# Kernel tuning notes

Hardware: AMD Instinct MI355X
Metric: run time of the kernel (lower is better)

The kernel has to match this reference:

```python
import jax, jax.numpy as jnp
import numpy as np

B, S, D, H, F, E, K = 2, 2048, 1024, 16, 4096, 8, 2
DK = D // H


def _ln(x, g, b, eps=1e-5):
    m = jnp.mean(x, axis=-1, keepdims=True)
    v = jnp.var(x, axis=-1, keepdims=True)
    return (x - m) * jax.lax.rsqrt(v + eps) * g + b


def _silu(x):
    return x * jax.nn.sigmoid(x)


def _gated_proj(x, w1, b1, w2, b2):
    # SiLU(x W1 + b1) * (x W2 + b2)
    return _silu(x @ w1 + b1) * (x @ w2 + b2)


def setup_inputs() -> dict:
    key = jax.random.key(0)
    ks = jax.random.split(key, 32)

    def n(k, shape, s=0.02):
        return jax.random.normal(k, shape, jnp.float32) * s

    inp = {
        "x": jax.random.normal(ks[0], (B, S, D), jnp.float32),
        "wq1": n(ks[1], (D, D)), "bq1": jnp.zeros((D,), jnp.float32),
        "wq2": n(ks[2], (D, D)), "bq2": jnp.zeros((D,), jnp.float32),
        "wk1": n(ks[3], (D, D)), "bk1": jnp.zeros((D,), jnp.float32),
        "wk2": n(ks[4], (D, D)), "bk2": jnp.zeros((D,), jnp.float32),
        "wv1": n(ks[5], (D, D)), "bv1": jnp.zeros((D,), jnp.float32),
        "wv2": n(ks[6], (D, D)), "bv2": jnp.zeros((D,), jnp.float32),
        "wo": n(ks[7], (D, D)), "bo": jnp.zeros((D,), jnp.float32),
        "ln1_g": jnp.ones((D,), jnp.float32), "ln1_b": jnp.zeros((D,), jnp.float32),
        "ln2_g": jnp.ones((D,), jnp.float32), "ln2_b": jnp.zeros((D,), jnp.float32),
        "gate_w": n(ks[8], (D, E)), "gate_b": jnp.zeros((E,), jnp.float32),
        "e_w1": n(ks[9], (E, D, F)), "e_b1": jnp.zeros((E, F), jnp.float32),
        "e_w2": n(ks[10], (E, F, D)), "e_b2": jnp.zeros((E, D), jnp.float32),
        "e_w3": n(ks[11], (E, D, F)), "e_b3": jnp.zeros((E, F), jnp.float32),
    }
    return inp


def _attention(x2, wq1, bq1, wq2, bq2, wk1, bk1, wk2, bk2,
               wv1, bv1, wv2, bv2, wo, bo, eps=1e-6):
    q = _gated_proj(x2, wq1, bq1, wq2, bq2).reshape(B, S, H, DK)
    k = _gated_proj(x2, wk1, bk1, wk2, bk2).reshape(B, S, H, DK)
    v = _gated_proj(x2, wv1, bv1, wv2, bv2).reshape(B, S, H, DK)
    phi_q = jax.nn.elu(q) + 1.0
    phi_k = jax.nn.elu(k) + 1.0
    # kv: [B,H,DK,DK] -- associative reordering of linear attention
    kv = jnp.einsum("bshd,bshe->bhde", phi_k, v)
    ksum = jnp.sum(phi_k, axis=1)  # [B,H,DK]
    qksum = jnp.einsum("bshd,bhd->bsh", phi_q, ksum)
    num = jnp.einsum("bshd,bhde->bshe", phi_q, kv)
    out = num / (qksum[..., None] + eps)  # [B,S,H,DK]
    return out.reshape(B, S, D) @ wo + bo


def _moe(x2, gate_w, gate_b, e_w1, e_b1, e_w2, e_b2, e_w3, e_b3):
    gate_probs = jax.nn.softmax(x2 @ gate_w + gate_b, axis=-1)  # [B,S,E]
    topv, topi = jax.lax.top_k(gate_probs, K)  # [B,S,K]
    topv = topv / (jnp.sum(topv, axis=-1, keepdims=True) + 1e-6)
    # combine weight per expert: [B,S,E]
    comb = jnp.sum(jax.nn.one_hot(topi, E, dtype=x2.dtype) * topv[..., None], axis=-2)
    out = jnp.zeros_like(x2)
    for e in range(E):  # small fixed expert count
        h = _silu(x2 @ e_w1[e] + e_b1[e]) * (x2 @ e_w3[e] + e_b3[e])
        out = out + (h @ e_w2[e] + e_b2[e]) * comb[..., e, None]
    return out


def reference(x, wq1, bq1, wq2, bq2, wk1, bk1, wk2, bk2, wv1, bv1, wv2, bv2,
              wo, bo, ln1_g, ln1_b, ln2_g, ln2_b, gate_w, gate_b,
              e_w1, e_b1, e_w2, e_b2, e_w3, e_b3):
    x2 = _ln(x, ln1_g, ln1_b)
    x = x + _attention(x2, wq1, bq1, wq2, bq2, wk1, bk1, wk2, bk2,
                       wv1, bv1, wv2, bv2, wo, bo)
    x2 = _ln(x, ln2_g, ln2_b)
    x = x + _moe(x2, gate_w, gate_b, e_w1, e_b1, e_w2, e_b2, e_w3, e_b3)
    return x
```

## Files before the change

### kernel.cpp

```cpp
#include <hip/hip_runtime.h>
#include <cstdint>
#include <cstddef>

typedef __bf16 bf16;
typedef bf16  bf16x8 __attribute__((ext_vector_type(8)));
typedef bf16  bf16x4 __attribute__((ext_vector_type(4)));
typedef float f32x4  __attribute__((ext_vector_type(4)));

#define B_ 2
#define S_ 2048
#define D_ 1024
#define H_ 16
#define F_ 4096
#define E_ 8
#define T_ (B_*S_)

__device__ __forceinline__ void gl16(const bf16* g, bf16* l) {
    __builtin_amdgcn_global_load_lds(
        (const __attribute__((address_space(1))) void*)g,
        (__attribute__((address_space(3))) void*)l, 16, 0, 0);
}

__global__ __launch_bounds__(256) void transpose_convert(const float* __restrict__ in,
                                                         bf16* __restrict__ out,
                                                         int R, int C) {
    __shared__ float tile[32][33];
    size_t mat = blockIdx.z;
    in  += mat * (size_t)R * C;
    out += mat * (size_t)R * C;
    int c0 = blockIdx.x * 32, r0 = blockIdx.y * 32;
    for (int i = threadIdx.y; i < 32; i += 8)
        tile[i][threadIdx.x] = in[(size_t)(r0 + i) * C + c0 + threadIdx.x];
    __syncthreads();
    for (int i = threadIdx.y; i < 32; i += 8)
        out[(size_t)(c0 + i) * R + r0 + threadIdx.x] = (bf16)tile[threadIdx.x][i];
}

__global__ __launch_bounds__(256) void ln_kernel(const float* __restrict__ xin,
                                                 const float* __restrict__ gam,
                                                 const float* __restrict__ bet,
                                                 bf16* __restrict__ obf,
                                                 float* __restrict__ of32) {
    int row = blockIdx.x, tid = threadIdx.x;
    const float4* xr = (const float4*)(xin + (size_t)row * D_);
    float4 v = xr[tid];
    float s  = v.x + v.y + v.z + v.w;
    float s2 = v.x*v.x + v.y*v.y + v.z*v.z + v.w*v.w;
    #pragma unroll
    for (int o = 1; o < 64; o <<= 1) { s += __shfl_xor(s, o); s2 += __shfl_xor(s2, o); }
    __shared__ float red[8];
    int wave = tid >> 6, lane = tid & 63;
    if (lane == 0) { red[wave] = s; red[4 + wave] = s2; }
    __syncthreads();
    s  = red[0] + red[1] + red[2] + red[3];
    s2 = red[4] + red[5] + red[6] + red[7];
    float m   = s * (1.0f / D_);
    float var = s2 * (1.0f / D_) - m * m;
    float rs  = rsqrtf(var + 1e-5f);
    float4 gv = ((const float4*)gam)[tid];
    float4 bv = ((const float4*)bet)[tid];
    float y0 = (v.x - m) * rs * gv.x + bv.x;
    float y1 = (v.y - m) * rs * gv.y + bv.y;
    float y2 = (v.z - m) * rs * gv.z + bv.z;
    float y3 = (v.w - m) * rs * gv.w + bv.w;
    bf16x4 ov; ov[0] = (bf16)y0; ov[1] = (bf16)y1; ov[2] = (bf16)y2; ov[3] = (bf16)y3;
    *(bf16x4*)(obf + (size_t)row * D_ + tid * 4) = ov;
    if (of32) {
        float4 o4; o4.x = y0; o4.y = y1; o4.z = y2; o4.w = y3;
        ((float4*)of32)[(size_t)row * (D_/4) + tid] = o4;
    }
}


template<int MODE>
__global__ __launch_bounds__(256) void gemm_dual128(const bf16* __restrict__ A,
                                                    const bf16* __restrict__ B1,
                                                    const bf16* __restrict__ B2,
                                                    const float* __restrict__ bias1,
                                                    const float* __restrict__ bias2,
                                                    float* __restrict__ out,
                                                    int N, int K) {
    __shared__ alignas(16) bf16 As [128 * 32];
    __shared__ alignas(16) bf16 B1s[64 * 32];
    __shared__ alignas(16) bf16 B2s[64 * 32];
    const int tid = threadIdx.x;
    const int wave = tid >> 6, lane = tid & 63;
    const int nb = blockIdx.x, mb = blockIdx.y;
    const int wr = (wave >> 1) * 64;
    const int wc = (wave & 1) * 32;
    const int fr = lane & 15, fk = (lane >> 4) * 8;
    const int srow = lane >> 2;
    const int scol = (lane & 3) * 8;
    const int cA0 = wave, cA1 = wave + 4;
    const bf16* Ap0 = A  + (size_t)(mb * 128 + cA0 * 16 + srow) * K + scol;
    const bf16* Ap1 = A  + (size_t)(mb * 128 + cA1 * 16 + srow) * K + scol;
    const bf16* B1p = B1 + (size_t)(nb * 64 + wave * 16 + srow) * K + scol;
    const bf16* B2p = B2 + (size_t)(nb * 64 + wave * 16 + srow) * K + scol;
    bf16* lA0 = As  + cA0 * 512;
    bf16* lA1 = As  + cA1 * 512;
    bf16* lB1 = B1s + wave * 512;
    bf16* lB2 = B2s + wave * 512;
    f32x4 acc1[4][2] = {};
    f32x4 acc2[4][2] = {};
    for (int k0 = 0; k0 < K; k0 += 32) {
        gl16(Ap0 + k0, lA0);
        gl16(Ap1 + k0, lA1);
        gl16(B1p + k0, lB1);
        gl16(B2p + k0, lB2);
        __syncthreads();
        bf16x8 af[4];
        #pragma unroll
        for (int mi = 0; mi < 4; mi++)
            af[mi] = *(const bf16x8*)&As[(wr + mi * 16 + fr) * 32 + fk];
        #pragma unroll
        for (int ni = 0; ni < 2; ni++) {
            bf16x8 b1f = *(const bf16x8*)&B1s[(wc + ni * 16 + fr) * 32 + fk];
            bf16x8 b2f = *(const bf16x8*)&B2s[(wc + ni * 16 + fr) * 32 + fk];
            #pragma unroll
            for (int mi = 0; mi < 4; mi++) {
                acc1[mi][ni] = __builtin_amdgcn_mfma_f32_16x16x32_bf16(af[mi], b1f, acc1[mi][ni], 0, 0, 0);
                acc2[mi][ni] = __builtin_amdgcn_mfma_f32_16x16x32_bf16(af[mi], b2f, acc2[mi][ni], 0, 0, 0);
            }
        }
        __syncthreads();
    }
    const int col = lane & 15, rowq = (lane >> 4) * 4;
    #pragma unroll
    for (int ni = 0; ni < 2; ni++) {
        int gn = nb * 64 + wc + ni * 16 + col;
        float bb1 = bias1[gn], bb2 = bias2[gn];
        #pragma unroll
        for (int mi = 0; mi < 4; mi++) {
            #pragma unroll
            for (int r = 0; r < 4; r++) {
                int gm = mb * 128 + wr + mi * 16 + rowq + r;
                float p1 = acc1[mi][ni][r] + bb1;
                float p2 = acc2[mi][ni][r] + bb2;
                float g = (p1 / (1.0f + expf(-p1))) * p2;
                size_t idx = (size_t)gm * N + gn;
                if (MODE == 0) {
                    float e = g > 0.0f ? g : expm1f(g);
                    out[idx] = e + 1.0f;
                } else {
                    out[idx] = g;
                }
            }
        }
    }
}

__global__ __launch_bounds__(256) void gemm_single128(const bf16* __restrict__ A,
                                                      const bf16* __restrict__ Bt,
                                                      float* __restrict__ out,
                                                      int N, int K) {
    __shared__ alignas(16) bf16 As[128 * 32];
    __shared__ alignas(16) bf16 Bs[64 * 32];
    const int tid = threadIdx.x;
    const int wave = tid >> 6, lane = tid & 63;
    const int nb = blockIdx.x, mb = blockIdx.y;
    const int wr = (wave >> 1) * 64, wc = (wave & 1) * 32;
    const int fr = lane & 15, fk = (lane >> 4) * 8;
    const int srow = lane >> 2, scol = (lane & 3) * 8;
    const int cA0 = wave, cA1 = wave + 4;
    const bf16* Ap0 = A  + (size_t)(mb * 128 + cA0 * 16 + srow) * K + scol;
    const bf16* Ap1 = A  + (size_t)(mb * 128 + cA1 * 16 + srow) * K + scol;
    const bf16* Bp  = Bt + (size_t)(nb * 64 + wave * 16 + srow) * K + scol;
    bf16* lA0 = As + cA0 * 512;
    bf16* lA1 = As + cA1 * 512;
    bf16* lB  = Bs + wave * 512;
    f32x4 acc[4][2] = {};
    for (int k0 = 0; k0 < K; k0 += 32) {
        gl16(Ap0 + k0, lA0);
        gl16(Ap1 + k0, lA1);
        gl16(Bp  + k0, lB);
        __syncthreads();
        bf16x8 af[4];
        #pragma unroll
        for (int mi = 0; mi < 4; mi++)
            af[mi] = *(const bf16x8*)&As[(wr + mi * 16 + fr) * 32 + fk];
        #pragma unroll
        for (int ni = 0; ni < 2; ni++) {
            bf16x8 bf = *(const bf16x8*)&Bs[(wc + ni * 16 + fr) * 32 + fk];
            #pragma unroll
            for (int mi = 0; mi < 4; mi++)
                acc[mi][ni] = __builtin_amdgcn_mfma_f32_16x16x32_bf16(af[mi], bf, acc[mi][ni], 0, 0, 0);
        }
        __syncthreads();
    }
    const int col = lane & 15, rowq = (lane >> 4) * 4;
    #pragma unroll
    for (int ni = 0; ni < 2; ni++) {
        int gn = nb * 64 + wc + ni * 16 + col;
        #pragma unroll
        for (int mi = 0; mi < 4; mi++)
            #pragma unroll
            for (int r = 0; r < 4; r++) {
                int gm = mb * 128 + wr + mi * 16 + rowq + r;
                out[(size_t)gm * N + gn] = acc[mi][ni][r];
            }
    }
}

__global__ __launch_bounds__(256) void gemm_dual_moe128(const bf16* __restrict__ A,
                                                        const bf16* __restrict__ B1all,
                                                        const bf16* __restrict__ B2all,
                                                        const float* __restrict__ b1all,
                                                        const float* __restrict__ b2all,
                                                        const int* __restrict__ list,
                                                        const int* __restrict__ counts,
                                                        const int* __restrict__ ebase,
                                                        bf16* __restrict__ outAct,
                                                        int N, int K) {
    const int e = blockIdx.z;
    const int cnt = counts[e * 64];
    const int mb = blockIdx.y;
    if (mb * 128 >= cnt) return;
    __shared__ alignas(16) bf16 As [128 * 32];
    __shared__ alignas(16) bf16 B1s[64 * 32];
    __shared__ alignas(16) bf16 B2s[64 * 32];
    const bf16* B1 = B1all + (size_t)e * N * K;
    const bf16* B2 = B2all + (size_t)e * N * K;
    const float* bias1 = b1all + (size_t)e * N;
    const float* bias2 = b2all + (size_t)e * N;
    const int tid = threadIdx.x;
    const int wave = tid >> 6, lane = tid & 63;
    const int nb = blockIdx.x;
    const int wr = (wave >> 1) * 64, wc = (wave & 1) * 32;
    const int fr = lane & 15, fk = (lane >> 4) * 8;
    const int srow = lane >> 2, scol = (lane & 3) * 8;
    const int cA0 = wave, cA1 = wave + 4;
    int gr0 = mb * 128 + cA0 * 16 + srow;
    int gr1 = mb * 128 + cA1 * 16 + srow;
    int tok0 = list[e * T_ + (gr0 < cnt ? gr0 : cnt - 1)];
    int tok1 = list[e * T_ + (gr1 < cnt ? gr1 : cnt - 1)];
    const bf16* Ap0 = A  + (size_t)tok0 * K + scol;
    const bf16* Ap1 = A  + (size_t)tok1 * K + scol;
    const bf16* B1p = B1 + (size_t)(nb * 64 + wave * 16 + srow) * K + scol;
    const bf16* B2p = B2 + (size_t)(nb * 64 + wave * 16 + srow) * K + scol;
    bf16* lA0 = As  + cA0 * 512;
    bf16* lA1 = As  + cA1 * 512;
    bf16* lB1 = B1s + wave * 512;
    bf16* lB2 = B2s + wave * 512;
    f32x4 acc1[4][2] = {};
    f32x4 acc2[4][2] = {};
    for (int k0 = 0; k0 < K; k0 += 32) {
        gl16(Ap0 + k0, lA0);
        gl16(Ap1 + k0, lA1);
        gl16(B1p + k0, lB1);
        gl16(B2p + k0, lB2);
        __syncthreads();
        bf16x8 af[4];
        #pragma unroll
        for (int mi = 0; mi < 4; mi++)
            af[mi] = *(const bf16x8*)&As[(wr + mi * 16 + fr) * 32 + fk];
        #pragma unroll
        for (int ni = 0; ni < 2; ni++) {
            bf16x8 b1f = *(const bf16x8*)&B1s[(wc + ni * 16 + fr) * 32 + fk];
            bf16x8 b2f = *(const bf16x8*)&B2s[(wc + ni * 16 + fr) * 32 + fk];
            #pragma unroll
            for (int mi = 0; mi < 4; mi++) {
                acc1[mi][ni] = __builtin_amdgcn_mfma_f32_16x16x32_bf16(af[mi], b1f, acc1[mi][ni], 0, 0, 0);
                acc2[mi][ni] = __builtin_amdgcn_mfma_f32_16x16x32_bf16(af[mi], b2f, acc2[mi][ni], 0, 0, 0);
            }
        }
        __syncthreads();
    }
    const int col = lane & 15, rowq = (lane >> 4) * 4;
    const size_t rbase = (size_t)ebase[e] + mb * 128;
    #pragma unroll
    for (int ni = 0; ni < 2; ni++) {
        int gn = nb * 64 + wc + ni * 16 + col;
        float bb1 = bias1[gn], bb2 = bias2[gn];
        #pragma unroll
        for (int mi = 0; mi < 4; mi++)
            #pragma unroll
            for (int r = 0; r < 4; r++) {
                int lm = wr + mi * 16 + rowq + r;
                float p1 = acc1[mi][ni][r] + bb1;
                float p2 = acc2[mi][ni][r] + bb2;
                float g = (p1 / (1.0f + expf(-p1))) * p2;
                outAct[(rbase + lm) * N + gn] = (bf16)g;
            }
    }
}

__global__ __launch_bounds__(256) void gemm_down_moe128(const bf16* __restrict__ Act,
                                                        const bf16* __restrict__ Ball,
                                                        const float* __restrict__ ball,
                                                        const int* __restrict__ list,
                                                        const float* __restrict__ wgt,
                                                        const int* __restrict__ counts,
                                                        const int* __restrict__ ebase,
                                                        float* __restrict__ out,
                                                        int N, int K) {
    const int e = blockIdx.z;
    const int cnt = counts[e * 64];
    const int mb = blockIdx.y;
    if (mb * 128 >= cnt) return;
    __shared__ alignas(16) bf16 As[128 * 32];
    __shared__ alignas(16) bf16 Bs[64 * 32];
    const bf16* A  = Act + (size_t)ebase[e] * K;
    const bf16* Bt = Ball + (size_t)e * N * K;
    const float* bias = ball + (size_t)e * N;
    const int tid = threadIdx.x;
    const int wave = tid >> 6, lane = tid & 63;
    const int nb = blockIdx.x;
    const int wr = (wave >> 1) * 64, wc = (wave & 1) * 32;
    const int fr = lane & 15, fk = (lane >> 4) * 8;
    const int srow = lane >> 2, scol = (lane & 3) * 8;
    const int cA0 = wave, cA1 = wave + 4;
    const bf16* Ap0 = A  + (size_t)(mb * 128 + cA0 * 16 + srow) * K + scol;
    const bf16* Ap1 = A  + (size_t)(mb * 128 + cA1 * 16 + srow) * K + scol;
    const bf16* Bp  = Bt + (size_t)(nb * 64 + wave * 16 + srow) * K + scol;
    bf16* lA0 = As + cA0 * 512;
    bf16* lA1 = As + cA1 * 512;
    bf16* lB  = Bs + wave * 512;
    f32x4 acc[4][2] = {};
    for (int k0 = 0; k0 < K; k0 += 32) {
        gl16(Ap0 + k0, lA0);
        gl16(Ap1 + k0, lA1);
        gl16(Bp  + k0, lB);
        __syncthreads();
        bf16x8 af[4];
        #pragma unroll
        for (int mi = 0; mi < 4; mi++)
            af[mi] = *(const bf16x8*)&As[(wr + mi * 16 + fr) * 32 + fk];
        #pragma unroll
        for (int ni = 0; ni < 2; ni++) {
            bf16x8 bf = *(const bf16x8*)&Bs[(wc + ni * 16 + fr) * 32 + fk];
            #pragma unroll
            for (int mi = 0; mi < 4; mi++)
                acc[mi][ni] = __builtin_amdgcn_mfma_f32_16x16x32_bf16(af[mi], bf, acc[mi][ni], 0, 0, 0);
        }
        __syncthreads();
    }
    const int col = lane & 15, rowq = (lane >> 4) * 4;
    #pragma unroll
    for (int ni = 0; ni < 2; ni++) {
        int gn = nb * 64 + wc + ni * 16 + col;
        float bb = bias[gn];
        #pragma unroll
        for (int mi = 0; mi < 4; mi++)
            #pragma unroll
            for (int r = 0; r < 4; r++) {
                int gm = mb * 128 + wr + mi * 16 + rowq + r;
                if (gm < cnt) {
                    int tok = list[e * T_ + gm];
                    float w = wgt[e * T_ + gm];
                    atomicAdd(&out[(size_t)tok * N + gn], (acc[mi][ni][r] + bb) * w);
                }
            }
    }
}

__global__ __launch_bounds__(256) void attn_kv_part(const float* __restrict__ phi_k,
                                                    const float* __restrict__ vv_g,
                                                    float* __restrict__ kvp,
                                                    float* __restrict__ ksp) {
    int bh = blockIdx.x;
    int chunk = blockIdx.y;
    int b = bh >> 4, h = bh & 15;
    __shared__ float pk[64][68];
    __shared__ float vv[64][68];
    int tid = threadIdx.x;
    int d0 = (tid >> 4) * 4;
    int e0 = (tid & 15) * 4;
    float acc[4][4] = {};
    float ks[4] = {};
    int sbeg = chunk * (S_ / 8);
    for (int s0 = sbeg; s0 < sbeg + S_ / 8; s0 += 64) {
        __syncthreads();
        for (int i = tid; i < 1024; i += 256) {
            int r = i >> 4, c4 = i & 15;
            size_t base = ((size_t)(b * S_ + s0 + r) * D_ + h * 64);
            ((float4*)&pk[r][0])[c4] = ((const float4*)(phi_k + base))[c4];
            ((float4*)&vv[r][0])[c4] = ((const float4*)(vv_g + base))[c4];
        }
        __syncthreads();
        for (int s = 0; s < 64; s++) {
            float a0 = pk[s][d0], a1 = pk[s][d0+1], a2 = pk[s][d0+2], a3 = pk[s][d0+3];
            float b0 = vv[s][e0], b1 = vv[s][e0+1], b2 = vv[s][e0+2], b3 = vv[s][e0+3];
            acc[0][0] += a0*b0; acc[0][1] += a0*b1; acc[0][2] += a0*b2; acc[0][3] += a0*b3;
            acc[1][0] += a1*b0; acc[1][1] += a1*b1; acc[1][2] += a1*b2; acc[1][3] += a1*b3;
            acc[2][0] += a2*b0; acc[2][1] += a2*b1; acc[2][2] += a2*b2; acc[2][3] += a2*b3;
            acc[3][0] += a3*b0; acc[3][1] += a3*b1; acc[3][2] += a3*b2; acc[3][3] += a3*b3;
            if ((tid & 15) == 0) { ks[0] += a0; ks[1] += a1; ks[2] += a2; ks[3] += a3; }
        }
    }
    float* kvo = kvp + ((size_t)bh * 8 + chunk) * 4096;
    for (int i = 0; i < 4; i++)
        for (int j = 0; j < 4; j++)
            kvo[(d0 + i) * 64 + e0 + j] = acc[i][j];
    if ((tid & 15) == 0)
        for (int i = 0; i < 4; i++) ksp[((size_t)bh * 8 + chunk) * 64 + d0 + i] = ks[i];
}

__global__ __launch_bounds__(256) void attn_kv_reduce(const float* __restrict__ kvp,
                                                      const float* __restrict__ ksp,
                                                      float* __restrict__ kv,
                                                      float* __restrict__ ksum) {
    int bh = blockIdx.x;
    int tid = threadIdx.x;
    #pragma unroll
    for (int i = 0; i < 4; i++) {
        int idx = i * 256 + tid;
        float4 s = {0, 0, 0, 0};
        #pragma unroll
        for (int c = 0; c < 8; c++) {
            float4 p = ((const float4*)(kvp + ((size_t)bh * 8 + c) * 4096))[idx];
            s.x += p.x; s.y += p.y; s.z += p.z; s.w += p.w;
        }
        ((float4*)(kv + (size_t)bh * 4096))[idx] = s;
    }
    if (tid < 64) {
        float s = 0;
        #pragma unroll
        for (int c = 0; c < 8; c++) s += ksp[((size_t)bh * 8 + c) * 64 + tid];
        ksum[bh * 64 + tid] = s;
    }
}

__global__ __launch_bounds__(256) void attn_num(const float* __restrict__ phi_q,
                                                const float* __restrict__ kv,
                                                const float* __restrict__ ksum,
                                                bf16* __restrict__ outb) {
    int bh = blockIdx.y;
    int b = bh >> 4, h = bh & 15;
    int s0 = blockIdx.x * 64;
    __shared__ float kvs[64][64];
    __shared__ float pqs[64][68];
    __shared__ float kss[64];
    int tid = threadIdx.x;
    const float* kvsrc = kv + (size_t)bh * 4096;
    for (int i = tid; i < 1024; i += 256) ((float4*)kvs)[i] = ((const float4*)kvsrc)[i];
    if (tid < 16) ((float4*)kss)[tid] = ((const float4*)(ksum + bh * 64))[tid];
    for (int i = tid; i < 1024; i += 256) {
        int r = i >> 4, c4 = i & 15;
        ((float4*)&pqs[r][0])[c4] =
            ((const float4*)(phi_q + ((size_t)(b * S_ + s0 + r) * D_ + h * 64)))[c4];
    }
    __syncthreads();
    int tok = tid >> 2;
    int e0  = (tid & 3) * 16;
    float acc[16] = {};
    float qk = 0.0f;
    for (int d = 0; d < 64; d++) {
        float pq = pqs[tok][d];
        qk += pq * kss[d];
        #pragma unroll
        for (int ei = 0; ei < 16; ei++) acc[ei] += pq * kvs[d][e0 + ei];
    }
    float inv = 1.0f / (qk + 1e-6f);
    int t = b * S_ + s0 + tok;
    bf16* op = outb + (size_t)t * D_ + h * 64 + e0;
    #pragma unroll
    for (int ei = 0; ei < 16; ei++) op[ei] = (bf16)(acc[ei] * inv);
}

__global__ __launch_bounds__(256) void residual_kernel(const float* __restrict__ x,
                                                       const float* __restrict__ prod,
                                                       const float* __restrict__ bo,
                                                       float* __restrict__ x1,
                                                       float* __restrict__ outp) {
    int i = blockIdx.x * 256 + threadIdx.x;
    float4 xv = ((const float4*)x)[i];
    float4 pv = ((const float4*)prod)[i];
    float4 bv = ((const float4*)bo)[i & 255];
    float4 r;
    r.x = xv.x + pv.x + bv.x; r.y = xv.y + pv.y + bv.y;
    r.z = xv.z + pv.z + bv.z; r.w = xv.w + pv.w + bv.w;
    ((float4*)x1)[i] = r;
    ((float4*)outp)[i] = r;
}

__global__ void zero_counts(int* counts) {
    counts[threadIdx.x] = 0;
}

__global__ void expert_bases(const int* __restrict__ counts, int* __restrict__ ebase) {
    if (threadIdx.x == 0) {
        int b = 0;
        #pragma unroll
        for (int e = 0; e < E_; e++) {
            ebase[e] = b;
            b += (counts[e * 64] + 127) & ~127;
        }
    }
}

__global__ __launch_bounds__(256) void gate_kernel(const float* __restrict__ x2f,
                                                   const float* __restrict__ gw,
                                                   const float* __restrict__ gb,
                                                   int* __restrict__ counts,
                                                   int* __restrict__ list,
                                                   float* __restrict__ wgt) {
    int tid = threadIdx.x;
    int wave = tid >> 6, lane = tid & 63;
    int t = blockIdx.x * 4 + wave;
    const float* xr = x2f + (size_t)t * D_;
    float le[8] = {};
    for (int i = 0; i < 16; i++) {
        int d = lane + i * 64;
        float xv = xr[d];
        const float4* g4 = (const float4*)(gw + (size_t)d * 8);
        float4 a = g4[0], b = g4[1];
        le[0] += xv * a.x; le[1] += xv * a.y; le[2] += xv * a.z; le[3] += xv * a.w;
        le[4] += xv * b.x; le[5] += xv * b.y; le[6] += xv * b.z; le[7] += xv * b.w;
    }
    #pragma unroll
    for (int o = 1; o < 64; o <<= 1)
        #pragma unroll
        for (int e = 0; e < 8; e++) le[e] += __shfl_xor(le[e], o);
    if (lane == 0) {
        float probs[8]; float mx = -1e30f;
        for (int e = 0; e < 8; e++) { le[e] += gb[e]; mx = fmaxf(mx, le[e]); }
        float s = 0.0f;
        for (int e = 0; e < 8; e++) { probs[e] = expf(le[e] - mx); s += probs[e]; }
        float invs = 1.0f / s;
        for (int e = 0; e < 8; e++) probs[e] *= invs;
        int i1 = 0; float v1 = probs[0];
        for (int e = 1; e < 8; e++) if (probs[e] > v1) { v1 = probs[e]; i1 = e; }
        int i2 = -1; float v2 = -1.0f;
        for (int e = 0; e < 8; e++) if (e != i1 && probs[e] > v2) { v2 = probs[e]; i2 = e; }
        float inv = 1.0f / (v1 + v2 + 1e-6f);
        int p1 = atomicAdd(&counts[i1 * 64], 1);
        list[i1 * T_ + p1] = t; wgt[i1 * T_ + p1] = v1 * inv;
        int p2 = atomicAdd(&counts[i2 * 64], 1);
        list[i2 * T_ + p2] = t; wgt[i2 * T_ + p2] = v2 * inv;
    }
}

extern "C" void kernel_launch(void* const* d_in, const int* in_sizes, int n_in,
                              void* d_out, int out_size, void* d_ws, size_t ws_size,
                              hipStream_t stream) {
    const float* x    = (const float*)d_in[0];
    const float* wq1  = (const float*)d_in[1];
    const float* bq1  = (const float*)d_in[2];
    const float* wq2  = (const float*)d_in[3];
    const float* bq2  = (const float*)d_in[4];
    const float* wk1  = (const float*)d_in[5];
    const float* bk1  = (const float*)d_in[6];
    const float* wk2  = (const float*)d_in[7];
    const float* bk2  = (const float*)d_in[8];
    const float* wv1  = (const float*)d_in[9];
    const float* bv1  = (const float*)d_in[10];
    const float* wv2  = (const float*)d_in[11];
    const float* bv2  = (const float*)d_in[12];
    const float* wo   = (const float*)d_in[13];
    const float* bo   = (const float*)d_in[14];
    const float* ln1g = (const float*)d_in[15];
    const float* ln1b = (const float*)d_in[16];
    const float* ln2g = (const float*)d_in[17];
    const float* ln2b = (const float*)d_in[18];
    const float* gw   = (const float*)d_in[19];
    const float* gb   = (const float*)d_in[20];
    const float* ew1  = (const float*)d_in[21];
    const float* eb1  = (const float*)d_in[22];
    const float* ew2  = (const float*)d_in[23];
    const float* eb2  = (const float*)d_in[24];
    const float* ew3  = (const float*)d_in[25];
    const float* eb3  = (const float*)d_in[26];
    float* out = (float*)d_out;

    char* wsb = (char*)d_ws;
    size_t off = 0;
    auto carve = [&](size_t bytes) -> char* {
        char* r = wsb + off;
        off = (off + bytes + 255) & ~(size_t)255;
        return r;
    };
    bf16* Wq1t = (bf16*)carve((size_t)D_ * D_ * 2);
    bf16* Wq2t = (bf16*)carve((size_t)D_ * D_ * 2);
    bf16* Wk1t = (bf16*)carve((size_t)D_ * D_ * 2);
    bf16* Wk2t = (bf16*)carve((size_t)D_ * D_ * 2);
    bf16* Wv1t = (bf16*)carve((size_t)D_ * D_ * 2);
    bf16* Wv2t = (bf16*)carve((size_t)D_ * D_ * 2);
    bf16* Wot  = (bf16*)carve((size_t)D_ * D_ * 2);
    bf16* We1t = (bf16*)carve((size_t)E_ * D_ * F_ * 2);
    bf16* We3t = (bf16*)carve((size_t)E_ * D_ * F_ * 2);
    bf16* We2t = (bf16*)carve((size_t)E_ * D_ * F_ * 2);
    bf16*  X2b  = (bf16*)carve((size_t)T_ * D_ * 2);
    float* PhiQ = (float*)carve((size_t)T_ * D_ * 4);
    float* PhiK = (float*)carve((size_t)T_ * D_ * 4);
    float* Vb   = (float*)carve((size_t)T_ * D_ * 4);
    float* KV   = (float*)carve((size_t)B_ * H_ * 64 * 64 * 4);
    float* KS   = (float*)carve((size_t)B_ * H_ * 64 * 4);
    float* KVp  = (float*)carve((size_t)B_ * H_ * 8 * 64 * 64 * 4);
    float* KSp  = (float*)carve((size_t)B_ * H_ * 8 * 64 * 4);
    bf16*  Attn = (bf16*)carve((size_t)T_ * D_ * 2);
    float* WoP  = (float*)carve((size_t)T_ * D_ * 4);
    float* X1   = (float*)carve((size_t)T_ * D_ * 4);
    bf16*  X2c  = (bf16*)carve((size_t)T_ * D_ * 2);
    int*   Cnt  = (int*)carve((size_t)E_ * 64 * 4);
    int*   List = (int*)carve((size_t)E_ * T_ * 4);
    float* Wgt  = (float*)carve((size_t)E_ * T_ * 4);
    int*   Ebase = (int*)carve((size_t)E_ * 4);
    bf16*  Act  = (bf16*)PhiQ;
    float* X2f  = WoP;

    dim3 tb32(32, 8);
    transpose_convert<<<dim3(32, 32, 1), tb32, 0, stream>>>(wq1, Wq1t, D_, D_);
    transpose_convert<<<dim3(32, 32, 1), tb32, 0, stream>>>(wq2, Wq2t, D_, D_);
    transpose_convert<<<dim3(32, 32, 1), tb32, 0, stream>>>(wk1, Wk1t, D_, D_);
    transpose_convert<<<dim3(32, 32, 1), tb32, 0, stream>>>(wk2, Wk2t, D_, D_);
    transpose_convert<<<dim3(32, 32, 1), tb32, 0, stream>>>(wv1, Wv1t, D_, D_);
    transpose_convert<<<dim3(32, 32, 1), tb32, 0, stream>>>(wv2, Wv2t, D_, D_);
    transpose_convert<<<dim3(32, 32, 1), tb32, 0, stream>>>(wo,  Wot,  D_, D_);
    transpose_convert<<<dim3(F_/32, D_/32, E_), tb32, 0, stream>>>(ew1, We1t, D_, F_);
    transpose_convert<<<dim3(F_/32, D_/32, E_), tb32, 0, stream>>>(ew3, We3t, D_, F_);
    transpose_convert<<<dim3(D_/32, F_/32, E_), tb32, 0, stream>>>(ew2, We2t, F_, D_);

    zero_counts<<<1, E_ * 64, 0, stream>>>(Cnt);

    ln_kernel<<<T_, 256, 0, stream>>>(x, ln1g, ln1b, X2b, nullptr);

    gemm_dual128<0><<<dim3(D_/64, T_/128), 256, 0, stream>>>(X2b, Wq1t, Wq2t, bq1, bq2, PhiQ, D_, D_);
    gemm_dual128<0><<<dim3(D_/64, T_/128), 256, 0, stream>>>(X2b, Wk1t, Wk2t, bk1, bk2, PhiK, D_, D_);
    gemm_dual128<1><<<dim3(D_/64, T_/128), 256, 0, stream>>>(X2b, Wv1t, Wv2t, bv1, bv2, Vb,   D_, D_);

    attn_kv_part<<<dim3(B_ * H_, 8), 256, 0, stream>>>(PhiK, Vb, KVp, KSp);
    attn_kv_reduce<<<B_ * H_, 256, 0, stream>>>(KVp, KSp, KV, KS);
    attn_num<<<dim3(S_/64, B_ * H_), 256, 0, stream>>>(PhiQ, KV, KS, Attn);

    gemm_single128<<<dim3(D_/64, T_/128), 256, 0, stream>>>(Attn, Wot, WoP, D_, D_);
    residual_kernel<<<T_ * D_ / 1024, 256, 0, stream>>>(x, WoP, bo, X1, out);

    ln_kernel<<<T_, 256, 0, stream>>>(X1, ln2g, ln2b, X2c, X2f);
    gate_kernel<<<T_ / 4, 256, 0, stream>>>(X2f, gw, gb, Cnt, List, Wgt);
    expert_bases<<<1, 64, 0, stream>>>(Cnt, Ebase);

    gemm_dual_moe128<<<dim3(F_/64, T_/128, E_), 256, 0, stream>>>(
        X2c, We1t, We3t, eb1, eb3, List, Cnt, Ebase, Act, F_, D_);
    gemm_down_moe128<<<dim3(D_/64, T_/128, E_), 256, 0, stream>>>(
        Act, We2t, eb2, List, Wgt, Cnt, Ebase, out, D_, F_);
}
```

Baseline: 1.153 ms.

## Double-buffer LDS in all GEMMs and widen single-B GEMM tiles to 128x128

```diff
diff --git a/kernel.cpp b/kernel.cpp
--- a/kernel.cpp
+++ b/kernel.cpp
@@ -80,42 +80,43 @@
                                                     const float* __restrict__ bias2,
                                                     float* __restrict__ out,
                                                     int N, int K) {
-    __shared__ alignas(16) bf16 As [128 * 32];
-    __shared__ alignas(16) bf16 B1s[64 * 32];
-    __shared__ alignas(16) bf16 B2s[64 * 32];
+    __shared__ alignas(16) bf16 As [2][128 * 32];
+    __shared__ alignas(16) bf16 B1s[2][64 * 32];
+    __shared__ alignas(16) bf16 B2s[2][64 * 32];
     const int tid = threadIdx.x;
     const int wave = tid >> 6, lane = tid & 63;
     const int nb = blockIdx.x, mb = blockIdx.y;
     const int wr = (wave >> 1) * 64;
     const int wc = (wave & 1) * 32;
     const int fr = lane & 15, fk = (lane >> 4) * 8;
-    const int srow = lane >> 2;
-    const int scol = (lane & 3) * 8;
-    const int cA0 = wave, cA1 = wave + 4;
-    const bf16* Ap0 = A  + (size_t)(mb * 128 + cA0 * 16 + srow) * K + scol;
-    const bf16* Ap1 = A  + (size_t)(mb * 128 + cA1 * 16 + srow) * K + scol;
+    const int srow = lane >> 2, scol = (lane & 3) * 8;
+    const int co = wave * 512;
+    const bf16* Ap0 = A  + (size_t)(mb * 128 + wave * 16 + srow) * K + scol;
+    const bf16* Ap1 = A  + (size_t)(mb * 128 + (wave + 4) * 16 + srow) * K + scol;
     const bf16* B1p = B1 + (size_t)(nb * 64 + wave * 16 + srow) * K + scol;
     const bf16* B2p = B2 + (size_t)(nb * 64 + wave * 16 + srow) * K + scol;
-    bf16* lA0 = As  + cA0 * 512;
-    bf16* lA1 = As  + cA1 * 512;
-    bf16* lB1 = B1s + wave * 512;
-    bf16* lB2 = B2s + wave * 512;
     f32x4 acc1[4][2] = {};
     f32x4 acc2[4][2] = {};
-    for (int k0 = 0; k0 < K; k0 += 32) {
-        gl16(Ap0 + k0, lA0);
-        gl16(Ap1 + k0, lA1);
-        gl16(B1p + k0, lB1);
-        gl16(B2p + k0, lB2);
-        __syncthreads();
+    gl16(Ap0, &As[0][co]);
+    gl16(Ap1, &As[0][co + 2048]);
+    gl16(B1p, &B1s[0][co]);
+    gl16(B2p, &B2s[0][co]);
+    __syncthreads();
+    int cur = 0;
+    for (int k0 = 32; k0 < K; k0 += 32) {
+        int nxt = cur ^ 1;
+        gl16(Ap0 + k0, &As[nxt][co]);
+        gl16(Ap1 + k0, &As[nxt][co + 2048]);
+        gl16(B1p + k0, &B1s[nxt][co]);
+        gl16(B2p + k0, &B2s[nxt][co]);
         bf16x8 af[4];
         #pragma unroll
         for (int mi = 0; mi < 4; mi++)
-            af[mi] = *(const bf16x8*)&As[(wr + mi * 16 + fr) * 32 + fk];
+            af[mi] = *(const bf16x8*)&As[cur][(wr + mi * 16 + fr) * 32 + fk];
         #pragma unroll
         for (int ni = 0; ni < 2; ni++) {
-            bf16x8 b1f = *(const bf16x8*)&B1s[(wc + ni * 16 + fr) * 32 + fk];
-            bf16x8 b2f = *(const bf16x8*)&B2s[(wc + ni * 16 + fr) * 32 + fk];
+            bf16x8 b1f = *(const bf16x8*)&B1s[cur][(wc + ni * 16 + fr) * 32 + fk];
+            bf16x8 b2f = *(const bf16x8*)&B2s[cur][(wc + ni * 16 + fr) * 32 + fk];
             #pragma unroll
             for (int mi = 0; mi < 4; mi++) {
                 acc1[mi][ni] = __builtin_amdgcn_mfma_f32_16x16x32_bf16(af[mi], b1f, acc1[mi][ni], 0, 0, 0);
@@ -123,6 +124,23 @@
             }
         }
         __syncthreads();
+        cur = nxt;
+    }
+    {
+        bf16x8 af[4];
+        #pragma unroll
+        for (int mi = 0; mi < 4; mi++)
+            af[mi] = *(const bf16x8*)&As[cur][(wr + mi * 16 + fr) * 32 + fk];
+        #pragma unroll
+        for (int ni = 0; ni < 2; ni++) {
+            bf16x8 b1f = *(const bf16x8*)&B1s[cur][(wc + ni * 16 + fr) * 32 + fk];
+            bf16x8 b2f = *(const bf16x8*)&B2s[cur][(wc + ni * 16 + fr) * 32 + fk];
+            #pragma unroll
+            for (int mi = 0; mi < 4; mi++) {
+                acc1[mi][ni] = __builtin_amdgcn_mfma_f32_16x16x32_bf16(af[mi], b1f, acc1[mi][ni], 0, 0, 0);
+                acc2[mi][ni] = __builtin_amdgcn_mfma_f32_16x16x32_bf16(af[mi], b2f, acc2[mi][ni], 0, 0, 0);
+            }
+        }
     }
     const int col = lane & 15, rowq = (lane >> 4) * 4;
     #pragma unroll
@@ -153,44 +171,65 @@
                                                       const bf16* __restrict__ Bt,
                                                       float* __restrict__ out,
                                                       int N, int K) {
-    __shared__ alignas(16) bf16 As[128 * 32];
-    __shared__ alignas(16) bf16 Bs[64 * 32];
+    __shared__ alignas(16) bf16 As[2][128 * 32];
+    __shared__ alignas(16) bf16 Bs[2][128 * 32];
     const int tid = threadIdx.x;
     const int wave = tid >> 6, lane = tid & 63;
     const int nb = blockIdx.x, mb = blockIdx.y;
-    const int wr = (wave >> 1) * 64, wc = (wave & 1) * 32;
+    const int wr = (wave >> 1) * 64, wc = (wave & 1) * 64;
     const int fr = lane & 15, fk = (lane >> 4) * 8;
     const int srow = lane >> 2, scol = (lane & 3) * 8;
-    const int cA0 = wave, cA1 = wave + 4;
-    const bf16* Ap0 = A  + (size_t)(mb * 128 + cA0 * 16 + srow) * K + scol;
-    const bf16* Ap1 = A  + (size_t)(mb * 128 + cA1 * 16 + srow) * K + scol;
-    const bf16* Bp  = Bt + (size_t)(nb * 64 + wave * 16 + srow) * K + scol;
-    bf16* lA0 = As + cA0 * 512;
-    bf16* lA1 = As + cA1 * 512;
-    bf16* lB  = Bs + wave * 512;
-    f32x4 acc[4][2] = {};
-    for (int k0 = 0; k0 < K; k0 += 32) {
-        gl16(Ap0 + k0, lA0);
-        gl16(Ap1 + k0, lA1);
-        gl16(Bp  + k0, lB);
+    const int co = wave * 512;
+    const bf16* Ap0 = A  + (size_t)(mb * 128 + wave * 16 + srow) * K + scol;
+    const bf16* Ap1 = A  + (size_t)(mb * 128 + (wave + 4) * 16 + srow) * K + scol;
+    const bf16* Bp0 = Bt + (size_t)(nb * 128 + wave * 16 + srow) * K + scol;
+    const bf16* Bp1 = Bt + (size_t)(nb * 128 + (wave + 4) * 16 + srow) * K + scol;
+    f32x4 acc[4][4] = {};
+    gl16(Ap0, &As[0][co]);
+    gl16(Ap1, &As[0][co + 2048]);
+    gl16(Bp0, &Bs[0][co]);
+    gl16(Bp1, &Bs[0][co + 2048]);
+    __syncthreads();
+    int cur = 0;
+    for (int k0 = 32; k0 < K; k0 += 32) {
+        int nxt = cur ^ 1;
+        gl16(Ap0 + k0, &As[nxt][co]);
+        gl16(Ap1 + k0, &As[nxt][co + 2048]);
+        gl16(Bp0 + k0, &Bs[nxt][co]);
+        gl16(Bp1 + k0, &Bs[nxt][co + 2048]);
+        bf16x8 af[4], bf[4];
+        #pragma unroll
+        for (int mi = 0; mi < 4; mi++)
+            af[mi] = *(const bf16x8*)&As[cur][(wr + mi * 16 + fr) * 32 + fk];
+        #pragma unroll
+        for (int ni = 0; ni < 4; ni++)
+            bf[ni] = *(const bf16x8*)&Bs[cur][(wc + ni * 16 + fr) * 32 + fk];
+        #pragma unroll
+        for (int ni = 0; ni < 4; ni++)
+            #pragma unroll
+            for (int mi = 0; mi < 4; mi++)
+                acc[mi][ni] = __builtin_amdgcn_mfma_f32_16x16x32_bf16(af[mi], bf[ni], acc[mi][ni], 0, 0, 0);
         __syncthreads();
-        bf16x8 af[4];
-        #pragma unroll
-        for (int mi = 0; mi < 4; mi++)
-            af[mi] = *(const bf16x8*)&As[(wr + mi * 16 + fr) * 32 + fk];
-        #pragma unroll
-        for (int ni = 0; ni < 2; ni++) {
-            bf16x8 bf = *(const bf16x8*)&Bs[(wc + ni * 16 + fr) * 32 + fk];
+        cur = nxt;
+    }
+    {
+        bf16x8 af[4], bf[4];
+        #pragma unroll
+        for (int mi = 0; mi < 4; mi++)
+            af[mi] = *(const bf16x8*)&As[cur][(wr + mi * 16 + fr) * 32 + fk];
+        #pragma unroll
+        for (int ni = 0; ni < 4; ni++)
+            bf[ni] = *(const bf16x8*)&Bs[cur][(wc + ni * 16 + fr) * 32 + fk];
+        #pragma unroll
+        for (int ni = 0; ni < 4; ni++)
             #pragma unroll
             for (int mi = 0; mi < 4; mi++)
-                acc[mi][ni] = __builtin_amdgcn_mfma_f32_16x16x32_bf16(af[mi], bf, acc[mi][ni], 0, 0, 0);
-        }
-        __syncthreads();
+                acc[mi][ni] = __builtin_amdgcn_mfma_f32_16x16x32_bf16(af[mi], bf[ni], acc[mi][ni], 0, 0, 0);
     }
     const int col = lane & 15, rowq = (lane >> 4) * 4;
     #pragma unroll
-    for (int ni = 0; ni < 2; ni++) {
-        int gn = nb * 64 + wc + ni * 16 + col;
+    for (int ni = 0; ni < 4; ni++) {
+        int gn = nb * 128 + wc + ni * 16 + col;
         #pragma unroll
         for (int mi = 0; mi < 4; mi++)
             #pragma unroll
@@ -215,9 +254,9 @@
     const int cnt = counts[e * 64];
     const int mb = blockIdx.y;
     if (mb * 128 >= cnt) return;
-    __shared__ alignas(16) bf16 As [128 * 32];
-    __shared__ alignas(16) bf16 B1s[64 * 32];
-    __shared__ alignas(16) bf16 B2s[64 * 32];
+    __shared__ alignas(16) bf16 As [2][128 * 32];
+    __shared__ alignas(16) bf16 B1s[2][64 * 32];
+    __shared__ alignas(16) bf16 B2s[2][64 * 32];
     const bf16* B1 = B1all + (size_t)e * N * K;
     const bf16* B2 = B2all + (size_t)e * N * K;
     const float* bias1 = b1all + (size_t)e * N;
@@ -228,35 +267,37 @@
     const int wr = (wave >> 1) * 64, wc = (wave & 1) * 32;
     const int fr = lane & 15, fk = (lane >> 4) * 8;
     const int srow = lane >> 2, scol = (lane & 3) * 8;
-    const int cA0 = wave, cA1 = wave + 4;
-    int gr0 = mb * 128 + cA0 * 16 + srow;
-    int gr1 = mb * 128 + cA1 * 16 + srow;
+    const int co = wave * 512;
+    int gr0 = mb * 128 + wave * 16 + srow;
+    int gr1 = mb * 128 + (wave + 4) * 16 + srow;
     int tok0 = list[e * T_ + (gr0 < cnt ? gr0 : cnt - 1)];
     int tok1 = list[e * T_ + (gr1 < cnt ? gr1 : cnt - 1)];
     const bf16* Ap0 = A  + (size_t)tok0 * K + scol;
     const bf16* Ap1 = A  + (size_t)tok1 * K + scol;
     const bf16* B1p = B1 + (size_t)(nb * 64 + wave * 16 + srow) * K + scol;
     const bf16* B2p = B2 + (size_t)(nb * 64 + wave * 16 + srow) * K + scol;
-    bf16* lA0 = As  + cA0 * 512;
-    bf16* lA1 = As  + cA1 * 512;
-    bf16* lB1 = B1s + wave * 512;
-    bf16* lB2 = B2s + wave * 512;
     f32x4 acc1[4][2] = {};
     f32x4 acc2[4][2] = {};
-    for (int k0 = 0; k0 < K; k0 += 32) {
-        gl16(Ap0 + k0, lA0);
-        gl16(Ap1 + k0, lA1);
-        gl16(B1p + k0, lB1);
-        gl16(B2p + k0, lB2);
-        __syncthreads();
+    gl16(Ap0, &As[0][co]);
+    gl16(Ap1, &As[0][co + 2048]);
+    gl16(B1p, &B1s[0][co]);
+    gl16(B2p, &B2s[0][co]);
+    __syncthreads();
+    int cur = 0;
+    for (int k0 = 32; k0 < K; k0 += 32) {
+        int nxt = cur ^ 1;
+        gl16(Ap0 + k0, &As[nxt][co]);
+        gl16(Ap1 + k0, &As[nxt][co + 2048]);
+        gl16(B1p + k0, &B1s[nxt][co]);
+        gl16(B2p + k0, &B2s[nxt][co]);
         bf16x8 af[4];
         #pragma unroll
         for (int mi = 0; mi < 4; mi++)
-            af[mi] = *(const bf16x8*)&As[(wr + mi * 16 + fr) * 32 + fk];
+            af[mi] = *(const bf16x8*)&As[cur][(wr + mi * 16 + fr) * 32 + fk];
         #pragma unroll
         for (int ni = 0; ni < 2; ni++) {
-            bf16x8 b1f = *(const bf16x8*)&B1s[(wc + ni * 16 + fr) * 32 + fk];
-            bf16x8 b2f = *(const bf16x8*)&B2s[(wc + ni * 16 + fr) * 32 + fk];
+            bf16x8 b1f = *(const bf16x8*)&B1s[cur][(wc + ni * 16 + fr) * 32 + fk];
+            bf16x8 b2f = *(const bf16x8*)&B2s[cur][(wc + ni * 16 + fr) * 32 + fk];
             #pragma unroll
             for (int mi = 0; mi < 4; mi++) {
                 acc1[mi][ni] = __builtin_amdgcn_mfma_f32_16x16x32_bf16(af[mi], b1f, acc1[mi][ni], 0, 0, 0);
@@ -264,6 +305,23 @@
             }
         }
         __syncthreads();
+        cur = nxt;
+    }
+    {
+        bf16x8 af[4];
+        #pragma unroll
+        for (int mi = 0; mi < 4; mi++)
+            af[mi] = *(const bf16x8*)&As[cur][(wr + mi * 16 + fr) * 32 + fk];
+        #pragma unroll
+        for (int ni = 0; ni < 2; ni++) {
+            bf16x8 b1f = *(const bf16x8*)&B1s[cur][(wc + ni * 16 + fr) * 32 + fk];
+            bf16x8 b2f = *(const bf16x8*)&B2s[cur][(wc + ni * 16 + fr) * 32 + fk];
+            #pragma unroll
+            for (int mi = 0; mi < 4; mi++) {
+                acc1[mi][ni] = __builtin_amdgcn_mfma_f32_16x16x32_bf16(af[mi], b1f, acc1[mi][ni], 0, 0, 0);
+                acc2[mi][ni] = __builtin_amdgcn_mfma_f32_16x16x32_bf16(af[mi], b2f, acc2[mi][ni], 0, 0, 0);
+            }
+        }
     }
     const int col = lane & 15, rowq = (lane >> 4) * 4;
     const size_t rbase = (size_t)ebase[e] + mb * 128;
@@ -297,47 +355,68 @@
     const int cnt = counts[e * 64];
     const int mb = blockIdx.y;
     if (mb * 128 >= cnt) return;
-    __shared__ alignas(16) bf16 As[128 * 32];
-    __shared__ alignas(16) bf16 Bs[64 * 32];
+    __shared__ alignas(16) bf16 As[2][128 * 32];
+    __shared__ alignas(16) bf16 Bs[2][128 * 32];
     const bf16* A  = Act + (size_t)ebase[e] * K;
     const bf16* Bt = Ball + (size_t)e * N * K;
     const float* bias = ball + (size_t)e * N;
     const int tid = threadIdx.x;
     const int wave = tid >> 6, lane = tid & 63;
     const int nb = blockIdx.x;
-    const int wr = (wave >> 1) * 64, wc = (wave & 1) * 32;
+    const int wr = (wave >> 1) * 64, wc = (wave & 1) * 64;
     const int fr = lane & 15, fk = (lane >> 4) * 8;
     const int srow = lane >> 2, scol = (lane & 3) * 8;
-    const int cA0 = wave, cA1 = wave + 4;
-    const bf16* Ap0 = A  + (size_t)(mb * 128 + cA0 * 16 + srow) * K + scol;
-    const bf16* Ap1 = A  + (size_t)(mb * 128 + cA1 * 16 + srow) * K + scol;
-    const bf16* Bp  = Bt + (size_t)(nb * 64 + wave * 16 + srow) * K + scol;
-    bf16* lA0 = As + cA0 * 512;
-    bf16* lA1 = As + cA1 * 512;
-    bf16* lB  = Bs + wave * 512;
-    f32x4 acc[4][2] = {};
-    for (int k0 = 0; k0 < K; k0 += 32) {
-        gl16(Ap0 + k0, lA0);
-        gl16(Ap1 + k0, lA1);
-        gl16(Bp  + k0, lB);
+    const int co = wave * 512;
+    const bf16* Ap0 = A  + (size_t)(mb * 128 + wave * 16 + srow) * K + scol;
+    const bf16* Ap1 = A  + (size_t)(mb * 128 + (wave + 4) * 16 + srow) * K + scol;
+    const bf16* Bp0 = Bt + (size_t)(nb * 128 + wave * 16 + srow) * K + scol;
+    const bf16* Bp1 = Bt + (size_t)(nb * 128 + (wave + 4) * 16 + srow) * K + scol;
+    f32x4 acc[4][4] = {};
+    gl16(Ap0, &As[0][co]);
+    gl16(Ap1, &As[0][co + 2048]);
+    gl16(Bp0, &Bs[0][co]);
+    gl16(Bp1, &Bs[0][co + 2048]);
+    __syncthreads();
+    int cur = 0;
+    for (int k0 = 32; k0 < K; k0 += 32) {
+        int nxt = cur ^ 1;
+        gl16(Ap0 + k0, &As[nxt][co]);
+        gl16(Ap1 + k0, &As[nxt][co + 2048]);
+        gl16(Bp0 + k0, &Bs[nxt][co]);
+        gl16(Bp1 + k0, &Bs[nxt][co + 2048]);
+        bf16x8 af[4], bf[4];
+        #pragma unroll
+        for (int mi = 0; mi < 4; mi++)
+            af[mi] = *(const bf16x8*)&As[cur][(wr + mi * 16 + fr) * 32 + fk];
+        #pragma unroll
+        for (int ni = 0; ni < 4; ni++)
+            bf[ni] = *(const bf16x8*)&Bs[cur][(wc + ni * 16 + fr) * 32 + fk];
+        #pragma unroll
+        for (int ni = 0; ni < 4; ni++)
+            #pragma unroll
+            for (int mi = 0; mi < 4; mi++)
+                acc[mi][ni] = __builtin_amdgcn_mfma_f32_16x16x32_bf16(af[mi], bf[ni], acc[mi][ni], 0, 0, 0);
         __syncthreads();
-        bf16x8 af[4];
-        #pragma unroll
-        for (int mi = 0; mi < 4; mi++)
-            af[mi] = *(const bf16x8*)&As[(wr + mi * 16 + fr) * 32 + fk];
-        #pragma unroll
-        for (int ni = 0; ni < 2; ni++) {
-            bf16x8 bf = *(const bf16x8*)&Bs[(wc + ni * 16 + fr) * 32 + fk];
+        cur = nxt;
+    }
+    {
+        bf16x8 af[4], bf[4];
+        #pragma unroll
+        for (int mi = 0; mi < 4; mi++)
+            af[mi] = *(const bf16x8*)&As[cur][(wr + mi * 16 + fr) * 32 + fk];
+        #pragma unroll
+        for (int ni = 0; ni < 4; ni++)
+            bf[ni] = *(const bf16x8*)&Bs[cur][(wc + ni * 16 + fr) * 32 + fk];
+        #pragma unroll
+        for (int ni = 0; ni < 4; ni++)
             #pragma unroll
             for (int mi = 0; mi < 4; mi++)
-                acc[mi][ni] = __builtin_amdgcn_mfma_f32_16x16x32_bf16(af[mi], bf, acc[mi][ni], 0, 0, 0);
-        }
-        __syncthreads();
+                acc[mi][ni] = __builtin_amdgcn_mfma_f32_16x16x32_bf16(af[mi], bf[ni], acc[mi][ni], 0, 0, 0);
     }
     const int col = lane & 15, rowq = (lane >> 4) * 4;
     #pragma unroll
-    for (int ni = 0; ni < 2; ni++) {
-        int gn = nb * 64 + wc + ni * 16 + col;
+    for (int ni = 0; ni < 4; ni++) {
+        int gn = nb * 128 + wc + ni * 16 + col;
         float bb = bias[gn];
         #pragma unroll
         for (int mi = 0; mi < 4; mi++)
@@ -622,7 +701,7 @@
     attn_kv_reduce<<<B_ * H_, 256, 0, stream>>>(KVp, KSp, KV, KS);
     attn_num<<<dim3(S_/64, B_ * H_), 256, 0, stream>>>(PhiQ, KV, KS, Attn);
 
-    gemm_single128<<<dim3(D_/64, T_/128), 256, 0, stream>>>(Attn, Wot, WoP, D_, D_);
+    gemm_single128<<<dim3(D_/128, T_/128), 256, 0, stream>>>(Attn, Wot, WoP, D_, D_);
     residual_kernel<<<T_ * D_ / 1024, 256, 0, stream>>>(x, WoP, bo, X1, out);
 
     ln_kernel<<<T_, 256, 0, stream>>>(X1, ln2g, ln2b, X2c, X2f);
@@ -631,6 +710,6 @@
 
     gemm_dual_moe128<<<dim3(F_/64, T_/128, E_), 256, 0, stream>>>(
         X2c, We1t, We3t, eb1, eb3, List, Cnt, Ebase, Act, F_, D_);
-    gemm_down_moe128<<<dim3(D_/64, T_/128, E_), 256, 0, stream>>>(
+    gemm_down_moe128<<<dim3(D_/128, T_/128, E_), 256, 0, stream>>>(
         Act, We2t, eb2, List, Wgt, Cnt, Ebase, out, D_, F_);
 }
```

After: 1.159 ms. Within noise of the previous version (+0.5%).
